# Optimization experiments

Measured on AMD Instinct MI355X. Metric: run time of the kernel, lower is better.

Reference implementation:

```python
import jax, jax.numpy as jnp
import numpy as np

D_MODEL = 512
N_QUBITS = 10
N_LAYERS = 2
N_TOKENS = 16384
DIM = 2 ** N_QUBITS


def _rx(t):
    c = jnp.cos(t / 2) + 0j
    s = -1j * jnp.sin(t / 2)
    return jnp.stack([jnp.stack([c, s]), jnp.stack([s, c])]).astype(jnp.complex64)


def _ry(t):
    c = jnp.cos(t / 2) + 0j
    s = jnp.sin(t / 2) + 0j
    return jnp.stack([jnp.stack([c, -s]), jnp.stack([s, c])]).astype(jnp.complex64)


def _rz(t):
    z = jnp.zeros((), jnp.complex64)
    return jnp.stack([jnp.stack([jnp.exp(-1j * t / 2), z]),
                      jnp.stack([z, jnp.exp(1j * t / 2)])]).astype(jnp.complex64)


def _apply_1q(state, q, U, n):
    # state: [B, 2^n]; qubit 0 is the most significant bit
    B = state.shape[0]
    s = state.reshape(B, 2 ** q, 2, 2 ** (n - q - 1))
    s = jnp.einsum('ij,bajk->baik', U, s)
    return s.reshape(B, 2 ** n)


def _simulate(psi, rot, ent, n):
    # psi: [B, 2^n] complex64. rot: [L, n, 3]. ent: [L, n-1].
    L = rot.shape[0]
    idx = jnp.arange(2 ** n)
    for l in range(L):
        for q in range(n):
            psi = _apply_1q(psi, q, _rx(rot[l, q, 0]), n)
            psi = _apply_1q(psi, q, _ry(rot[l, q, 1]), n)
            psi = _apply_1q(psi, q, _rz(rot[l, q, 2]), n)
        for i in range(n - 1):  # nearest-neighbor parameterized CZ (controlled-phase)
            q1, q2 = i, i + 1
            both = (((idx >> (n - 1 - q1)) & 1) & ((idx >> (n - 1 - q2)) & 1)) == 1
            phase = jnp.where(both, jnp.exp(1j * ent[l, i].astype(jnp.complex64)),
                              jnp.ones((), jnp.complex64))
            psi = psi * phase
    return psi


def setup_inputs() -> dict:
    key = jax.random.key(0)
    ks = jax.random.split(key, 6)
    return {
        'x': jax.random.normal(ks[0], (N_TOKENS, D_MODEL), jnp.float32),
        'W_in': jax.random.normal(ks[1], (DIM, D_MODEL), jnp.float32) / np.sqrt(D_MODEL),
        'b_in': jnp.zeros((DIM,), jnp.float32),
        'W_out': jax.random.normal(ks[2], (D_MODEL, DIM), jnp.float32) / np.sqrt(DIM),
        'b_out': jnp.zeros((D_MODEL,), jnp.float32),
        'rot': jax.random.normal(ks[3], (N_LAYERS, N_QUBITS, 3), jnp.float32),
        'ent': jax.random.normal(ks[4], (N_LAYERS, N_QUBITS - 1), jnp.float32),
        'ln_w': jnp.ones((D_MODEL,), jnp.float32),
        'ln_b': jnp.zeros((D_MODEL,), jnp.float32),
    }


def reference(x, W_in, b_in, W_out, b_out, rot, ent, ln_w, ln_b):
    n = rot.shape[1]
    # input projection to 2^n amplitudes, then L2-normalize (F.normalize, eps=1e-12)
    xq = x @ W_in.T + b_in
    norm = jnp.maximum(jnp.linalg.norm(xq, axis=-1, keepdims=True), 1e-12)
    psi = (xq / norm).astype(jnp.complex64)
    psi = _simulate(psi, rot, ent, n)
    probs = (psi.real ** 2 + psi.imag ** 2).astype(x.dtype)  # |amp|^2
    out = probs @ W_out.T + b_out
    # LayerNorm(d_model), eps=1e-5
    mu = jnp.mean(out, axis=-1, keepdims=True)
    var = jnp.mean((out - mu) ** 2, axis=-1, keepdims=True)
    return (out - mu) / jnp.sqrt(var + 1e-5) * ln_w + ln_b
```

## Files before the change

### kernel.cpp

```cpp
#include <hip/hip_runtime.h>
#include <cstdint>

#define TOKENS 16384
#define DMODEL 512
#define DIM    1024
#define NQ     10
#define NL     2
#define BM     128
#define BN     128
#define BK     32

typedef __bf16 bf16x8 __attribute__((ext_vector_type(8)));
typedef float  f32x4  __attribute__((ext_vector_type(4)));
typedef unsigned short u16x8 __attribute__((ext_vector_type(8)));

__device__ __forceinline__ float b2f(unsigned short h) {
    union { unsigned u; float f; } v; v.u = ((unsigned)h) << 16; return v.f;
}
__device__ __forceinline__ unsigned short f2b(float f) {
    unsigned u = __builtin_bit_cast(unsigned, f);
    return (unsigned short)((u + 0x7FFFu + ((u >> 16) & 1u)) >> 16);
}
__device__ __forceinline__ float2 cmul(float2 a, float2 b) {
    return make_float2(a.x * b.x - a.y * b.y, a.x * b.y + a.y * b.x);
}
__device__ __forceinline__ float2 cadd(float2 a, float2 b) {
    return make_float2(a.x + b.x, a.y + b.y);
}
__device__ __forceinline__ void async_copy16(const void* g, void* l) {
    __builtin_amdgcn_global_load_lds((const __attribute__((address_space(1))) void*)g,
                                     (__attribute__((address_space(3))) void*)l, 16, 0, 0);
}

__global__ __launch_bounds__(256)
void prep_all_kernel(const float* __restrict__ x,  unsigned short* __restrict__ xb,
                     const float* __restrict__ w2, unsigned short* __restrict__ w2b,
                     const float* __restrict__ W_in, unsigned short* __restrict__ wtT,
                     const float* __restrict__ rot, const float* __restrict__ ent,
                     const float* __restrict__ bin,
                     unsigned short* __restrict__ U, float* __restrict__ b2) {
    const int bid = blockIdx.x;
    const int t = threadIdx.x;

    if (bid < 256) {
        __shared__ float2 Gs[NL * NQ * 4];
        const int lane = t & 63;
        const int c = bid * 4 + (t >> 6);

        if (t < NL * NQ) {
            float tx = rot[t * 3 + 0] * 0.5f;
            float ty = rot[t * 3 + 1] * 0.5f;
            float tz = rot[t * 3 + 2] * 0.5f;
            float cx = cosf(tx), sx = sinf(tx);
            float cy = cosf(ty), sy = sinf(ty);
            float cz = cosf(tz), sz = sinf(tz);
            float2 rx00 = make_float2(cx, 0.f),  rx01 = make_float2(0.f, -sx);
            float2 rx10 = make_float2(0.f, -sx), rx11 = make_float2(cx, 0.f);
            float2 ry00 = make_float2(cy, 0.f),  ry01 = make_float2(-sy, 0.f);
            float2 ry10 = make_float2(sy, 0.f),  ry11 = make_float2(cy, 0.f);
            float2 m00 = cadd(cmul(ry00, rx00), cmul(ry01, rx10));
            float2 m01 = cadd(cmul(ry00, rx01), cmul(ry01, rx11));
            float2 m10 = cadd(cmul(ry10, rx00), cmul(ry11, rx10));
            float2 m11 = cadd(cmul(ry10, rx01), cmul(ry11, rx11));
            float2 e0 = make_float2(cz, -sz), e1 = make_float2(cz, sz);
            Gs[t * 4 + 0] = cmul(e0, m00);
            Gs[t * 4 + 1] = cmul(e0, m01);
            Gs[t * 4 + 2] = cmul(e1, m10);
            Gs[t * 4 + 3] = cmul(e1, m11);
        }
        float ef[NL * (NQ - 1)];
        #pragma unroll
        for (int i = 0; i < NL * (NQ - 1); i++) ef[i] = ent[i];
        __syncthreads();

        float2 amp[16];
        #pragma unroll
        for (int r = 0; r < 16; r++)
            amp[r] = make_float2((lane * 16 + r == c) ? 1.f : 0.f, 0.f);

        #pragma unroll 1
        for (int li = 0; li < NL; li++) {
            const int l = NL - 1 - li;
            #pragma unroll
            for (int r = 0; r < 16; r++) {
                int idx = lane * 16 + r;
                float ang = 0.f;
                #pragma unroll
                for (int q = 0; q < NQ - 1; q++) {
                    int both = ((idx >> (9 - q)) & 1) & ((idx >> (8 - q)) & 1);
                    if (both) ang += ef[l * (NQ - 1) + q];
                }
                amp[r] = cmul(amp[r], make_float2(cosf(ang), sinf(ang)));
            }
            const float2* Gl = Gs + l * NQ * 4;
            #pragma unroll
            for (int qq = 0; qq < NQ; qq++) {
                const int q = 9 - qq;
                float2 u00 = Gl[q * 4 + 0], u10 = Gl[q * 4 + 1];
                float2 u01 = Gl[q * 4 + 2], u11 = Gl[q * 4 + 3];
                if (q >= 6) {
                    const int S = 1 << (9 - q);
                    #pragma unroll
                    for (int r = 0; r < 16; r++) {
                        if (r & S) continue;
                        float2 a = amp[r], b = amp[r + S];
                        float2 n0, n1;
                        n0.x = u00.x * a.x - u00.y * a.y + u01.x * b.x - u01.y * b.y;
                        n0.y = u00.x * a.y + u00.y * a.x + u01.x * b.y + u01.y * b.x;
                        n1.x = u10.x * a.x - u10.y * a.y + u11.x * b.x - u11.y * b.y;
                        n1.y = u10.x * a.y + u10.y * a.x + u11.x * b.y + u11.y * b.x;
                        amp[r] = n0; amp[r + S] = n1;
                    }
                } else {
                    const int mask = 32 >> q;
                    int bit = (lane >> (5 - q)) & 1;
                    float2 ua = bit ? u11 : u00;
                    float2 ub = bit ? u10 : u01;
                    #pragma unroll
                    for (int r = 0; r < 16; r++) {
                        float px = __shfl_xor(amp[r].x, mask, 64);
                        float py = __shfl_xor(amp[r].y, mask, 64);
                        float nx = ua.x * amp[r].x - ua.y * amp[r].y + ub.x * px - ub.y * py;
                        float ny = ua.x * amp[r].y + ua.y * amp[r].x + ub.x * py + ub.y * px;
                        amp[r] = make_float2(nx, ny);
                    }
                }
            }
        }

        float accRe = 0.f, accIm = 0.f;
        #pragma unroll
        for (int i = 0; i < 4; i++) {
            float4 bv = *(const float4*)&bin[lane * 16 + i * 4];
            accRe += amp[i * 4 + 0].x * bv.x + amp[i * 4 + 1].x * bv.y
                   + amp[i * 4 + 2].x * bv.z + amp[i * 4 + 3].x * bv.w;
            accIm += amp[i * 4 + 0].y * bv.x + amp[i * 4 + 1].y * bv.y
                   + amp[i * 4 + 2].y * bv.z + amp[i * 4 + 3].y * bv.w;
        }
        #pragma unroll
        for (int m = 1; m < 64; m <<= 1) {
            accRe += __shfl_xor(accRe, m, 64);
            accIm += __shfl_xor(accIm, m, 64);
        }
        if (lane == 0) { b2[2 * c] = accRe; b2[2 * c + 1] = accIm; }

        u16x8 o0, o1, p0, p1;
        #pragma unroll
        for (int r = 0; r < 8; r++) {
            o0[r] = f2b(amp[r].x);     o1[r] = f2b(amp[r + 8].x);
            p0[r] = f2b(amp[r].y);     p1[r] = f2b(amp[r + 8].y);
        }
        unsigned short* rowRe = U + (size_t)(2 * c) * DIM + lane * 16;
        unsigned short* rowIm = U + (size_t)(2 * c + 1) * DIM + lane * 16;
        *(u16x8*)rowRe = o0; *(u16x8*)(rowRe + 8) = o1;
        *(u16x8*)rowIm = p0; *(u16x8*)(rowIm + 8) = p1;
        return;
    }

    if (bid < 768) {
        __shared__ float tile[32][33];
        const int b2i = bid - 256;
        const int tx = t & 31, ty = t >> 5;
        const int d0 = (b2i & 15) * 32, j0 = (b2i >> 4) * 32;
        #pragma unroll
        for (int i = 0; i < 32; i += 8)
            tile[ty + i][tx] = W_in[(size_t)(j0 + ty + i) * DMODEL + d0 + tx];
        __syncthreads();
        #pragma unroll
        for (int i = 0; i < 32; i += 8)
            wtT[(size_t)(d0 + ty + i) * DIM + j0 + tx] = f2b(tile[tx][ty + i]);
        return;
    }

    const int NX4 = TOKENS * DMODEL / 4;
    const int NW4 = DMODEL * DIM / 4;
    const int total = NX4 + NW4;
    const int stride = 2048 * 256;
    for (int i = (bid - 768) * 256 + t; i < total; i += stride) {
        const float* s; unsigned short* d; int j;
        if (i < NX4) { s = x;  d = xb;  j = i; }
        else         { s = w2; d = w2b; j = i - NX4; }
        float4 v = *(const float4*)&s[(size_t)j * 4];
        ushort4 o;
        o.x = f2b(v.x); o.y = f2b(v.y); o.z = f2b(v.z); o.w = f2b(v.w);
        *(ushort4*)&d[(size_t)j * 4] = o;
    }
}

__global__ __launch_bounds__(256)
void fold_kernel(const unsigned short* __restrict__ A, const unsigned short* __restrict__ B,
                 unsigned short* __restrict__ C) {
    __shared__ unsigned short lds_a[BM * BK];
    __shared__ unsigned short lds_b[BN * BK];
    const int t = threadIdx.x;
    const int wave = t >> 6, lane = t & 63;
    const int wm = wave >> 1, wn = wave & 1;
    const int bm0 = blockIdx.y * BM;
    const int bn0 = blockIdx.x * BN;
    const int K = DIM, N = DMODEL;

    f32x4 acc[4][4] = {};
    const int c0 = t, c1 = t + 256;
    const int r0 = c0 >> 2, g0 = (c0 & 3) ^ ((r0 >> 1) & 3);
    const int r1 = c1 >> 2, g1 = (c1 & 3) ^ ((r1 >> 1) & 3);

    for (int k0 = 0; k0 < K; k0 += BK) {
        async_copy16(A + (size_t)(bm0 + r0) * K + k0 + g0 * 8, (char*)lds_a + wave * 1024);
        async_copy16(A + (size_t)(bm0 + r1) * K + k0 + g1 * 8, (char*)lds_a + wave * 1024 + 4096);
        async_copy16(B + (size_t)(bn0 + r0) * K + k0 + g0 * 8, (char*)lds_b + wave * 1024);
        async_copy16(B + (size_t)(bn0 + r1) * K + k0 + g1 * 8, (char*)lds_b + wave * 1024 + 4096);
        __syncthreads();

        bf16x8 af[4], bfr[4];
        #pragma unroll
        for (int i = 0; i < 4; i++) {
            int row = wm * 64 + i * 16 + (lane & 15);
            int slot = (lane >> 4) ^ ((row >> 1) & 3);
            af[i] = *(const bf16x8*)&lds_a[row * BK + slot * 8];
            int nrow = wn * 64 + i * 16 + (lane & 15);
            int nslot = (lane >> 4) ^ ((nrow >> 1) & 3);
            bfr[i] = *(const bf16x8*)&lds_b[nrow * BK + nslot * 8];
        }
        #pragma unroll
        for (int i = 0; i < 4; i++)
            #pragma unroll
            for (int j = 0; j < 4; j++)
                acc[i][j] = __builtin_amdgcn_mfma_f32_16x16x32_bf16(af[i], bfr[j], acc[i][j], 0, 0, 0);
        __syncthreads();
    }

    #pragma unroll
    for (int i = 0; i < 4; i++)
        #pragma unroll
        for (int j = 0; j < 4; j++) {
            int col = bn0 + wn * 64 + j * 16 + (lane & 15);
            #pragma unroll
            for (int r = 0; r < 4; r++) {
                int row = bm0 + wm * 64 + i * 16 + (lane >> 4) * 4 + r;
                C[(size_t)row * N + col] = f2b(acc[i][j][r]);
            }
        }
}

__global__ __launch_bounds__(512, 2)
void gemm1_kernel(const unsigned short* __restrict__ A, const unsigned short* __restrict__ B,
                  const float* __restrict__ bias, unsigned short* __restrict__ P) {
    __shared__ unsigned short sm[2 * 32768];
    const int t = threadIdx.x;
    const int wave = t >> 6, lane = t & 63;
    const int wm = wave >> 2, wn = wave & 3;
    const int laneR = lane & 15;

    const int bid = blockIdx.x;
    const int swz = (bid & 7) * 64 + (bid >> 3);
    const int bm0 = (swz >> 3) * 256;
    const int bn0 = (swz & 7) * 256;

    const int csrc  = (t & 3) ^ ((t >> 3) & 3);
    const int rowg  = t >> 2;
    const unsigned aOff0 = (unsigned)(bm0 + rowg) * DMODEL + csrc * 8;
    const unsigned aOff1 = (unsigned)(bm0 + 128 + rowg) * DMODEL + csrc * 8;
    const unsigned bOff0 = (unsigned)(bn0 + rowg) * DMODEL + csrc * 8;
    const unsigned bOff1 = (unsigned)(bn0 + 128 + rowg) * DMODEL + csrc * 8;

    const int slotc = (((lane >> 4) ^ ((lane >> 1) & 3)) & 3) * 8;

    f32x4 acc[8][4] = {};

    #define G1_STAGE(nbuf, kk, kb)                                                 \
    {                                                                              \
        unsigned short* d0 = sm + (nbuf) * 32768 + (kk) * 8192 + wave * 512;       \
        async_copy16(A + aOff0 + (kb) + (kk) * 32, d0);                            \
        async_copy16(A + aOff1 + (kb) + (kk) * 32, d0 + 4096);                     \
        async_copy16(B + bOff0 + (kb) + (kk) * 32, d0 + 16384);                    \
        async_copy16(B + bOff1 + (kb) + (kk) * 32, d0 + 20480);                    \
    }

    #define G1_COMPUTE(cbuf, kk)                                                   \
    {                                                                              \
        const unsigned short* la = sm + (cbuf) * 32768 + (kk) * 8192;              \
        const unsigned short* lb = la + 16384;                                     \
        bf16x8 af[8], bfr[4];                                                      \
        _Pragma("unroll")                                                          \
        for (int i = 0; i < 8; i++)                                                \
            af[i] = *(const bf16x8*)&la[(wm * 128 + i * 16 + laneR) * 32 + slotc]; \
        _Pragma("unroll")                                                          \
        for (int j = 0; j < 4; j++)                                                \
            bfr[j] = *(const bf16x8*)&lb[(wn * 64 + j * 16 + laneR) * 32 + slotc]; \
        __builtin_amdgcn_s_setprio(1);                                             \
        _Pragma("unroll")                                                          \
        for (int i = 0; i < 8; i++)                                                \
            _Pragma("unroll")                                                      \
            for (int j = 0; j < 4; j++)                                            \
                acc[i][j] = __builtin_amdgcn_mfma_f32_16x16x32_bf16(af[i], bfr[j], acc[i][j], 0, 0, 0); \
        __builtin_amdgcn_s_setprio(0);                                             \
    }

    G1_STAGE(0, 0, 0);
    G1_STAGE(0, 1, 0);
    asm volatile("s_waitcnt vmcnt(4)" ::: "memory");
    asm volatile("s_barrier" ::: "memory");

    #pragma unroll
    for (int kt = 0; kt < 7; kt++) {
        const int cur = kt & 1, nxt = cur ^ 1;
        const unsigned kb = (unsigned)(kt + 1) * 64;
        G1_STAGE(nxt, 0, kb);
        G1_COMPUTE(cur, 0);
        asm volatile("s_waitcnt vmcnt(4)" ::: "memory");
        asm volatile("s_barrier" ::: "memory");
        G1_STAGE(nxt, 1, kb);
        G1_COMPUTE(cur, 1);
        asm volatile("s_waitcnt vmcnt(4)" ::: "memory");
        asm volatile("s_barrier" ::: "memory");
    }
    G1_COMPUTE(1, 0);
    asm volatile("s_waitcnt vmcnt(0)" ::: "memory");
    asm volatile("s_barrier" ::: "memory");
    G1_COMPUTE(1, 1);

    #undef G1_STAGE
    #undef G1_COMPUTE

    #pragma unroll
    for (int i = 0; i < 8; i++) {
        #pragma unroll
        for (int j = 0; j < 4; j++) {
            int col = bn0 + wn * 64 + j * 16 + laneR;
            float bv = bias[col];
            #pragma unroll
            for (int r = 0; r < 4; r++) {
                int row = bm0 + wm * 128 + i * 16 + (lane >> 4) * 4 + r;
                float val = acc[i][j][r] + bv;
                float v2 = val * val;
                float v2p = v2 + __shfl_xor(v2, 1, 64);
                if (!(lane & 1))
                    P[(size_t)row * DIM + (col >> 1)] = f2b(v2p);
            }
        }
    }
}

__global__ __launch_bounds__(256)
void gemm2_ln_kernel(const unsigned short* __restrict__ A,
                     const unsigned short* __restrict__ B,
                     const float* __restrict__ bias,
                     const float* __restrict__ lw, const float* __restrict__ lb,
                     float* __restrict__ out) {
    __shared__ unsigned short lds_a[32 * BK];
    __shared__ unsigned short lds_b[512 * BK];
    __shared__ float redS[4][32], redQ[4][32];
    __shared__ float muS[32], rsS[32], n2s[32];
    const int t = threadIdx.x, wave = t >> 6, lane = t & 63;
    const int bm0 = blockIdx.x * 32;

    f32x4 acc[2][8] = {};
    f32x4 accN[2] = {};
    bf16x8 ones;
    #pragma unroll
    for (int r = 0; r < 8; r++) ones[r] = (__bf16)1.0f;

    const int ra = t >> 2, ga = (t & 3) ^ ((ra >> 1) & 3);

    for (int k0 = 0; k0 < DIM; k0 += BK) {
        if (wave < 2)
            async_copy16(A + (size_t)(bm0 + ra) * DIM + k0 + ga * 8,
                         (char*)lds_a + wave * 1024);
        #pragma unroll
        for (int s = 0; s < 8; s++) {
            int c = t + s * 256;
            int r = c >> 2, g = (c & 3) ^ ((r >> 1) & 3);
            async_copy16(B + (size_t)r * DIM + k0 + g * 8,
                         (char*)lds_b + s * 4096 + wave * 1024);
        }
        __syncthreads();

        bf16x8 af[2], bfr[8];
        #pragma unroll
        for (int i = 0; i < 2; i++) {
            int row = i * 16 + (lane & 15);
            int slot = (lane >> 4) ^ ((row >> 1) & 3);
            af[i] = *(const bf16x8*)&lds_a[row * BK + slot * 8];
        }
        #pragma unroll
        for (int j = 0; j < 8; j++) {
            int nrow = wave * 128 + j * 16 + (lane & 15);
            int nslot = (lane >> 4) ^ ((nrow >> 1) & 3);
            bfr[j] = *(const bf16x8*)&lds_b[nrow * BK + nslot * 8];
        }
        #pragma unroll
        for (int i = 0; i < 2; i++)
            #pragma unroll
            for (int j = 0; j < 8; j++)
                acc[i][j] = __builtin_amdgcn_mfma_f32_16x16x32_bf16(af[i], bfr[j], acc[i][j], 0, 0, 0);
        if (wave == 0) {
            #pragma unroll
            for (int i = 0; i < 2; i++)
                accN[i] = __builtin_amdgcn_mfma_f32_16x16x32_bf16(af[i], ones, accN[i], 0, 0, 0);
        }
        __syncthreads();
    }

    if (wave == 0 && (lane & 15) == 0) {
        #pragma unroll
        for (int i = 0; i < 2; i++)
            #pragma unroll
            for (int r = 0; r < 4; r++)
                n2s[i * 16 + (lane >> 4) * 4 + r] = accN[i][r];
    }
    __syncthreads();

    const int colb = wave * 128;
    float nn[8];
    #pragma unroll
    for (int i = 0; i < 2; i++)
        #pragma unroll
        for (int r = 0; r < 4; r++) {
            int rl = i * 16 + (lane >> 4) * 4 + r;
            nn[i * 4 + r] = 1.0f / fmaxf(n2s[rl], 1e-24f);
        }
    float pS[8], pQ[8];
    #pragma unroll
    for (int i = 0; i < 2; i++)
        #pragma unroll
        for (int r = 0; r < 4; r++) {
            float s = 0.f, q = 0.f;
            #pragma unroll
            for (int j = 0; j < 8; j++) {
                int col = colb + j * 16 + (lane & 15);
                float val = acc[i][j][r] * nn[i * 4 + r] + bias[col];
                acc[i][j][r] = val;
                s += val; q += val * val;
            }
            s += __shfl_xor(s, 1, 64); q += __shfl_xor(q, 1, 64);
            s += __shfl_xor(s, 2, 64); q += __shfl_xor(q, 2, 64);
            s += __shfl_xor(s, 4, 64); q += __shfl_xor(q, 4, 64);
            s += __shfl_xor(s, 8, 64); q += __shfl_xor(q, 8, 64);
            pS[i * 4 + r] = s; pQ[i * 4 + r] = q;
        }
    if ((lane & 15) == 0) {
        #pragma unroll
        for (int i = 0; i < 2; i++)
            #pragma unroll
            for (int r = 0; r < 4; r++) {
                int rl = i * 16 + (lane >> 4) * 4 + r;
                redS[wave][rl] = pS[i * 4 + r];
                redQ[wave][rl] = pQ[i * 4 + r];
            }
    }
    __syncthreads();
    if (t < 32) {
        float s = redS[0][t] + redS[1][t] + redS[2][t] + redS[3][t];
        float q = redQ[0][t] + redQ[1][t] + redQ[2][t] + redQ[3][t];
        float mu = s * (1.0f / DMODEL);
        float var = q * (1.0f / DMODEL) - mu * mu;
        muS[t] = mu;
        rsS[t] = rsqrtf(var + 1e-5f);
    }
    __syncthreads();
    #pragma unroll
    for (int i = 0; i < 2; i++)
        #pragma unroll
        for (int j = 0; j < 8; j++) {
            int col = colb + j * 16 + (lane & 15);
            float w = lw[col], bb = lb[col];
            #pragma unroll
            for (int r = 0; r < 4; r++) {
                int rl = i * 16 + (lane >> 4) * 4 + r;
                out[(size_t)(bm0 + rl) * DMODEL + col] =
                    (acc[i][j][r] - muS[rl]) * rsS[rl] * w + bb;
            }
        }
}

extern "C" void kernel_launch(void* const* d_in, const int* in_sizes, int n_in,
                              void* d_out, int out_size, void* d_ws, size_t ws_size,
                              hipStream_t stream) {
    (void)in_sizes; (void)n_in; (void)out_size; (void)ws_size;
    const float* x     = (const float*)d_in[0];
    const float* W_in  = (const float*)d_in[1];
    const float* b_in  = (const float*)d_in[2];
    const float* W_out = (const float*)d_in[3];
    const float* b_out = (const float*)d_in[4];
    const float* rot   = (const float*)d_in[5];
    const float* ent   = (const float*)d_in[6];
    const float* ln_w  = (const float*)d_in[7];
    const float* ln_b  = (const float*)d_in[8];
    float* out = (float*)d_out;

    char* ws = (char*)d_ws;
    unsigned short* p    = (unsigned short*)ws;
    unsigned short* x_bf = (unsigned short*)(ws + 33554432ull);
    unsigned short* wtT  = (unsigned short*)(ws + 50331648ull);
    unsigned short* w2b  = (unsigned short*)(ws + 51380224ull);
    unsigned short* Ucat = (unsigned short*)(ws + 52428800ull);
    unsigned short* W1c  = (unsigned short*)(ws + 56623104ull);
    float*          b2   = (float*)(ws + 58720256ull);

    prep_all_kernel<<<2816, 256, 0, stream>>>(x, x_bf, W_out, w2b, W_in, wtT,
                                              rot, ent, b_in, Ucat, b2);
    fold_kernel<<<dim3(DMODEL / BN, 2 * DIM / BM), 256, 0, stream>>>(Ucat, wtT, W1c);
    gemm1_kernel<<<512, 512, 0, stream>>>(x_bf, W1c, b2, p);
    gemm2_ln_kernel<<<TOKENS / 32, 256, 0, stream>>>(
        p, w2b, b_out, ln_w, ln_b, out);
}
```

Measured before the change: 224.3 us.

## Restructure gemm1 main loop into four-quadrant ping-pong schedule with deeper prefetch

Rewrites the GEMM1 K-loop as eight 64-wide K tiles. Each tile is processed in four 4x2 MFMA quadrants, with LDS fragment loads interleaved between barriers, and global async loads for tile n+2 are issued into the buffer just consumed. The aim is to overlap LDS reads and global prefetch with MFMA work and to cut register pressure from holding all A/B fragments at once. In exchange it adds many more barriers per K step and adds fragile vmcnt bookkeeping.

After: 219.2 us. 1.02x faster.

```diff
diff --git a/kernel.cpp b/kernel.cpp
--- a/kernel.cpp
+++ b/kernel.cpp
@@ -256,8 +256,8 @@
     const int bm0 = (swz >> 3) * 256;
     const int bn0 = (swz & 7) * 256;
 
-    const int csrc  = (t & 3) ^ ((t >> 3) & 3);
-    const int rowg  = t >> 2;
+    const int csrc = (t & 3) ^ ((t >> 3) & 3);
+    const int rowg = t >> 2;
     const unsigned aOff0 = (unsigned)(bm0 + rowg) * DMODEL + csrc * 8;
     const unsigned aOff1 = (unsigned)(bm0 + 128 + rowg) * DMODEL + csrc * 8;
     const unsigned bOff0 = (unsigned)(bn0 + rowg) * DMODEL + csrc * 8;
@@ -267,60 +267,116 @@
 
     f32x4 acc[8][4] = {};
 
-    #define G1_STAGE(nbuf, kk, kb)                                                 \
-    {                                                                              \
-        unsigned short* d0 = sm + (nbuf) * 32768 + (kk) * 8192 + wave * 512;       \
-        async_copy16(A + aOff0 + (kb) + (kk) * 32, d0);                            \
-        async_copy16(A + aOff1 + (kb) + (kk) * 32, d0 + 4096);                     \
-        async_copy16(B + bOff0 + (kb) + (kk) * 32, d0 + 16384);                    \
-        async_copy16(B + bOff1 + (kb) + (kk) * 32, d0 + 20480);                    \
-    }
-
-    #define G1_COMPUTE(cbuf, kk)                                                   \
-    {                                                                              \
-        const unsigned short* la = sm + (cbuf) * 32768 + (kk) * 8192;              \
-        const unsigned short* lb = la + 16384;                                     \
-        bf16x8 af[8], bfr[4];                                                      \
-        _Pragma("unroll")                                                          \
-        for (int i = 0; i < 8; i++)                                                \
-            af[i] = *(const bf16x8*)&la[(wm * 128 + i * 16 + laneR) * 32 + slotc]; \
-        _Pragma("unroll")                                                          \
-        for (int j = 0; j < 4; j++)                                                \
-            bfr[j] = *(const bf16x8*)&lb[(wn * 64 + j * 16 + laneR) * 32 + slotc]; \
-        __builtin_amdgcn_s_setprio(1);                                             \
-        _Pragma("unroll")                                                          \
-        for (int i = 0; i < 8; i++)                                                \
-            _Pragma("unroll")                                                      \
-            for (int j = 0; j < 4; j++)                                            \
-                acc[i][j] = __builtin_amdgcn_mfma_f32_16x16x32_bf16(af[i], bfr[j], acc[i][j], 0, 0, 0); \
-        __builtin_amdgcn_s_setprio(0);                                             \
-    }
-
-    G1_STAGE(0, 0, 0);
-    G1_STAGE(0, 1, 0);
-    asm volatile("s_waitcnt vmcnt(4)" ::: "memory");
-    asm volatile("s_barrier" ::: "memory");
-
-    #pragma unroll
-    for (int kt = 0; kt < 7; kt++) {
-        const int cur = kt & 1, nxt = cur ^ 1;
-        const unsigned kb = (unsigned)(kt + 1) * 64;
-        G1_STAGE(nxt, 0, kb);
-        G1_COMPUTE(cur, 0);
-        asm volatile("s_waitcnt vmcnt(4)" ::: "memory");
-        asm volatile("s_barrier" ::: "memory");
-        G1_STAGE(nxt, 1, kb);
-        G1_COMPUTE(cur, 1);
-        asm volatile("s_waitcnt vmcnt(4)" ::: "memory");
-        asm volatile("s_barrier" ::: "memory");
-    }
-    G1_COMPUTE(1, 0);
-    asm volatile("s_waitcnt vmcnt(0)" ::: "memory");
-    asm volatile("s_barrier" ::: "memory");
-    G1_COMPUTE(1, 1);
-
-    #undef G1_STAGE
-    #undef G1_COMPUTE
+    #define STAGE_B4(nbuf, tile) {                                        \
+        unsigned short* d = sm + (nbuf) * 32768 + 16384 + wave * 512;     \
+        async_copy16(B + bOff0 + (tile) * 64,      d);                    \
+        async_copy16(B + bOff1 + (tile) * 64,      d + 4096);             \
+        async_copy16(B + bOff0 + (tile) * 64 + 32, d + 8192);             \
+        async_copy16(B + bOff1 + (tile) * 64 + 32, d + 12288);            \
+    }
+    #define STAGE_A4(nbuf, tile) {                                        \
+        unsigned short* d = sm + (nbuf) * 32768 + wave * 512;             \
+        async_copy16(A + aOff0 + (tile) * 64,      d);                    \
+        async_copy16(A + aOff1 + (tile) * 64,      d + 4096);             \
+        async_copy16(A + aOff0 + (tile) * 64 + 32, d + 8192);             \
+        async_copy16(A + aOff1 + (tile) * 64 + 32, d + 12288);            \
+    }
+    #define BARRIER()  asm volatile("s_barrier" ::: "memory")
+
+    STAGE_B4(0, 0); STAGE_A4(0, 0);
+    STAGE_B4(1, 1); STAGE_A4(1, 1);
+    asm volatile("s_waitcnt vmcnt(8)" ::: "memory");
+    BARRIER();
+
+    #pragma unroll
+    for (int n = 0; n < 8; n++) {
+        const int cb = n & 1;
+        const unsigned short* la = sm + cb * 32768;
+        const unsigned short* lb = la + 16384;
+        bf16x8 afv[4][2], bfv[4][2];
+
+        #pragma unroll
+        for (int kk = 0; kk < 2; kk++) {
+            #pragma unroll
+            for (int i = 0; i < 4; i++)
+                afv[i][kk] = *(const bf16x8*)&la[kk * 8192 + (wm * 128 + i * 16 + laneR) * 32 + slotc];
+            #pragma unroll
+            for (int j = 0; j < 2; j++)
+                bfv[j][kk] = *(const bf16x8*)&lb[kk * 8192 + (wn * 64 + j * 16 + laneR) * 32 + slotc];
+        }
+        BARRIER();
+        __builtin_amdgcn_sched_barrier(0);
+        __builtin_amdgcn_s_setprio(1);
+        #pragma unroll
+        for (int i = 0; i < 4; i++)
+            #pragma unroll
+            for (int j = 0; j < 2; j++)
+                #pragma unroll
+                for (int kk = 0; kk < 2; kk++)
+                    acc[i][j] = __builtin_amdgcn_mfma_f32_16x16x32_bf16(afv[i][kk], bfv[j][kk], acc[i][j], 0, 0, 0);
+        __builtin_amdgcn_s_setprio(0);
+        __builtin_amdgcn_sched_barrier(0);
+        BARRIER();
+
+        #pragma unroll
+        for (int kk = 0; kk < 2; kk++)
+            #pragma unroll
+            for (int j = 2; j < 4; j++)
+                bfv[j][kk] = *(const bf16x8*)&lb[kk * 8192 + (wn * 64 + j * 16 + laneR) * 32 + slotc];
+        BARRIER();
+        __builtin_amdgcn_sched_barrier(0);
+        __builtin_amdgcn_s_setprio(1);
+        #pragma unroll
+        for (int i = 0; i < 4; i++)
+            #pragma unroll
+            for (int j = 2; j < 4; j++)
+                #pragma unroll
+                for (int kk = 0; kk < 2; kk++)
+                    acc[i][j] = __builtin_amdgcn_mfma_f32_16x16x32_bf16(afv[i][kk], bfv[j][kk], acc[i][j], 0, 0, 0);
+        __builtin_amdgcn_s_setprio(0);
+        __builtin_amdgcn_sched_barrier(0);
+        BARRIER();
+
+        #pragma unroll
+        for (int kk = 0; kk < 2; kk++)
+            #pragma unroll
+            for (int i = 0; i < 4; i++)
+                afv[i][kk] = *(const bf16x8*)&la[kk * 8192 + (wm * 128 + 64 + i * 16 + laneR) * 32 + slotc];
+        if (n < 6) STAGE_B4(cb, n + 2);
+        BARRIER();
+        __builtin_amdgcn_sched_barrier(0);
+        __builtin_amdgcn_s_setprio(1);
+        #pragma unroll
+        for (int i = 0; i < 4; i++)
+            #pragma unroll
+            for (int j = 2; j < 4; j++)
+                #pragma unroll
+                for (int kk = 0; kk < 2; kk++)
+                    acc[4 + i][j] = __builtin_amdgcn_mfma_f32_16x16x32_bf16(afv[i][kk], bfv[j][kk], acc[4 + i][j], 0, 0, 0);
+        __builtin_amdgcn_s_setprio(0);
+        __builtin_amdgcn_sched_barrier(0);
+        BARRIER();
+
+        if (n < 6) STAGE_A4(cb, n + 2);
+        BARRIER();
+        __builtin_amdgcn_sched_barrier(0);
+        __builtin_amdgcn_s_setprio(1);
+        #pragma unroll
+        for (int i = 0; i < 4; i++)
+            #pragma unroll
+            for (int j = 0; j < 2; j++)
+                #pragma unroll
+                for (int kk = 0; kk < 2; kk++)
+                    acc[4 + i][j] = __builtin_amdgcn_mfma_f32_16x16x32_bf16(afv[i][kk], bfv[j][kk], acc[4 + i][j], 0, 0, 0);
+        __builtin_amdgcn_s_setprio(0);
+        __builtin_amdgcn_sched_barrier(0);
+        if (n < 6)      { asm volatile("s_waitcnt vmcnt(8)" ::: "memory"); }
+        else if (n == 6){ asm volatile("s_waitcnt vmcnt(0)" ::: "memory"); }
+        BARRIER();
+    }
+    #undef STAGE_A4
+    #undef STAGE_B4
+    #undef BARRIER
 
     #pragma unroll
     for (int i = 0; i < 8; i++) {
```

## Double-buffer gemm2 with async pipeline and split re/im rows for gemm1 epilogue

Applied to the files above, without the earlier changes.

Rewrites the second GEMM+LayerNorm kernel to process 64 rows per block with 512 threads and a double-buffered async-copy pipeline with explicit waitcnt/barriers, replacing the single-buffered loop that synchronized twice per K step. It also reorders the folded unitary rows so real and imaginary parts land 16 columns apart. This lets the gemm1 epilogue compute |amp|^2 within a lane instead of using a cross-lane shuffle and half-lane stores. The aim is to overlap global loads with MFMA work and cut epilogue shuffles, at the cost of more LDS per block and lower occupancy.

After: 202.5 us. 1.11x faster.

```diff
diff --git a/kernel.cpp b/kernel.cpp
--- a/kernel.cpp
+++ b/kernel.cpp
@@ -142,7 +142,8 @@
             accRe += __shfl_xor(accRe, m, 64);
             accIm += __shfl_xor(accIm, m, 64);
         }
-        if (lane == 0) { b2[2 * c] = accRe; b2[2 * c + 1] = accIm; }
+        const int nR = ((c >> 4) << 5) + (c & 15);
+        if (lane == 0) { b2[nR] = accRe; b2[nR + 16] = accIm; }
 
         u16x8 o0, o1, p0, p1;
         #pragma unroll
@@ -150,8 +151,8 @@
             o0[r] = f2b(amp[r].x);     o1[r] = f2b(amp[r + 8].x);
             p0[r] = f2b(amp[r].y);     p1[r] = f2b(amp[r + 8].y);
         }
-        unsigned short* rowRe = U + (size_t)(2 * c) * DIM + lane * 16;
-        unsigned short* rowIm = U + (size_t)(2 * c + 1) * DIM + lane * 16;
+        unsigned short* rowRe = U + (size_t)nR * DIM + lane * 16;
+        unsigned short* rowIm = U + (size_t)(nR + 16) * DIM + lane * 16;
         *(u16x8*)rowRe = o0; *(u16x8*)(rowRe + 8) = o1;
         *(u16x8*)rowIm = p0; *(u16x8*)(rowIm + 8) = p1;
         return;
@@ -245,6 +246,7 @@
 __global__ __launch_bounds__(512, 2)
 void gemm1_kernel(const unsigned short* __restrict__ A, const unsigned short* __restrict__ B,
                   const float* __restrict__ bias, unsigned short* __restrict__ P) {
+    const int K = DMODEL;
     __shared__ unsigned short sm[2 * 32768];
     const int t = threadIdx.x;
     const int wave = t >> 6, lane = t & 63;
@@ -256,8 +258,8 @@
     const int bm0 = (swz >> 3) * 256;
     const int bn0 = (swz & 7) * 256;
 
-    const int csrc  = (t & 3) ^ ((t >> 3) & 3);
-    const int rowg  = t >> 2;
+    const int csrc = (t & 3) ^ ((t >> 3) & 3);
+    const int rowg = t >> 2;
     const unsigned aOff0 = (unsigned)(bm0 + rowg) * DMODEL + csrc * 8;
     const unsigned aOff1 = (unsigned)(bm0 + 128 + rowg) * DMODEL + csrc * 8;
     const unsigned bOff0 = (unsigned)(bn0 + rowg) * DMODEL + csrc * 8;
@@ -301,6 +303,7 @@
     asm volatile("s_waitcnt vmcnt(4)" ::: "memory");
     asm volatile("s_barrier" ::: "memory");
 
+    const int NT = K / 64;
     #pragma unroll
     for (int kt = 0; kt < 7; kt++) {
         const int cur = kt & 1, nxt = cur ^ 1;
@@ -318,6 +321,7 @@
     asm volatile("s_waitcnt vmcnt(0)" ::: "memory");
     asm volatile("s_barrier" ::: "memory");
     G1_COMPUTE(1, 1);
+    (void)NT;
 
     #undef G1_STAGE
     #undef G1_COMPUTE
@@ -325,34 +329,41 @@
     #pragma unroll
     for (int i = 0; i < 8; i++) {
         #pragma unroll
-        for (int j = 0; j < 4; j++) {
-            int col = bn0 + wn * 64 + j * 16 + laneR;
-            float bv = bias[col];
+        for (int jp = 0; jp < 2; jp++) {
+            int colRe = bn0 + wn * 64 + jp * 32 + laneR;
+            float bRe = bias[colRe];
+            float bIm = bias[colRe + 16];
+            int pc = (bn0 >> 1) + wn * 32 + jp * 16 + laneR;
             #pragma unroll
             for (int r = 0; r < 4; r++) {
                 int row = bm0 + wm * 128 + i * 16 + (lane >> 4) * 4 + r;
-                float val = acc[i][j][r] + bv;
-                float v2 = val * val;
-                float v2p = v2 + __shfl_xor(v2, 1, 64);
-                if (!(lane & 1))
-                    P[(size_t)row * DIM + (col >> 1)] = f2b(v2p);
+                float vr = acc[i][2 * jp][r] + bRe;
+                float vi = acc[i][2 * jp + 1][r] + bIm;
+                P[(size_t)row * DIM + pc] = f2b(vr * vr + vi * vi);
             }
         }
     }
 }
 
-__global__ __launch_bounds__(256)
+__global__ __launch_bounds__(512)
 void gemm2_ln_kernel(const unsigned short* __restrict__ A,
                      const unsigned short* __restrict__ B,
                      const float* __restrict__ bias,
                      const float* __restrict__ lw, const float* __restrict__ lb,
                      float* __restrict__ out) {
-    __shared__ unsigned short lds_a[32 * BK];
-    __shared__ unsigned short lds_b[512 * BK];
-    __shared__ float redS[4][32], redQ[4][32];
-    __shared__ float muS[32], rsS[32], n2s[32];
+    __shared__ unsigned short sm[2 * 36864];
+    __shared__ float redS[4][64], redQ[4][64];
+    __shared__ float muS[64], rsS[64], n2s[64];
     const int t = threadIdx.x, wave = t >> 6, lane = t & 63;
-    const int bm0 = blockIdx.x * 32;
+    const int wm = wave >> 2, wn = wave & 3;
+    const int laneR = lane & 15;
+    const int bm0 = blockIdx.x * 64;
+
+    const int csrc = (t & 3) ^ ((t >> 3) & 3);
+    const int akk  = t >> 8, arow = (t >> 2) & 63;
+    const unsigned aSrc = (unsigned)(bm0 + arow) * DIM + akk * 32 + csrc * 8;
+    const int brow = t >> 2;
+    const int slotc = (((lane >> 4) ^ ((lane >> 1) & 3)) & 3) * 8;
 
     f32x4 acc[2][8] = {};
     f32x4 accN[2] = {};
@@ -360,75 +371,90 @@
     #pragma unroll
     for (int r = 0; r < 8; r++) ones[r] = (__bf16)1.0f;
 
-    const int ra = t >> 2, ga = (t & 3) ^ ((ra >> 1) & 3);
-
-    for (int k0 = 0; k0 < DIM; k0 += BK) {
-        if (wave < 2)
-            async_copy16(A + (size_t)(bm0 + ra) * DIM + k0 + ga * 8,
-                         (char*)lds_a + wave * 1024);
-        #pragma unroll
-        for (int s = 0; s < 8; s++) {
-            int c = t + s * 256;
-            int r = c >> 2, g = (c & 3) ^ ((r >> 1) & 3);
-            async_copy16(B + (size_t)r * DIM + k0 + g * 8,
-                         (char*)lds_b + s * 4096 + wave * 1024);
-        }
-        __syncthreads();
-
-        bf16x8 af[2], bfr[8];
-        #pragma unroll
-        for (int i = 0; i < 2; i++) {
-            int row = i * 16 + (lane & 15);
-            int slot = (lane >> 4) ^ ((row >> 1) & 3);
-            af[i] = *(const bf16x8*)&lds_a[row * BK + slot * 8];
-        }
-        #pragma unroll
-        for (int j = 0; j < 8; j++) {
-            int nrow = wave * 128 + j * 16 + (lane & 15);
-            int nslot = (lane >> 4) ^ ((nrow >> 1) & 3);
-            bfr[j] = *(const bf16x8*)&lds_b[nrow * BK + nslot * 8];
-        }
+    #define G2_STAGE_A(nbuf, kb) {                                          \
+        async_copy16(A + aSrc + (kb), sm + (nbuf) * 36864 + t * 8);         \
+    }
+    #define G2_STAGE_B(nbuf, kk, kb) {                                      \
+        unsigned short* d = sm + (nbuf) * 36864 + 4096 + (kk) * 16384 + t * 8; \
+        const unsigned short* s0 = B + (size_t)brow * DIM + (kb) + (kk) * 32 + csrc * 8; \
+        async_copy16(s0,                 d);                                 \
+        async_copy16(s0 + 128 * DIM,     d + 4096);                         \
+        async_copy16(s0 + 256 * DIM,     d + 8192);                         \
+        async_copy16(s0 + 384 * DIM,     d + 12288);                        \
+    }
+    #define G2_COMPUTE(cbuf, kk) {                                          \
+        const unsigned short* la  = sm + (cbuf) * 36864 + (kk) * 2048;      \
+        const unsigned short* lbp = sm + (cbuf) * 36864 + 4096 + (kk) * 16384; \
+        bf16x8 af[2], bfr[8];                                               \
+        _Pragma("unroll")                                                   \
+        for (int i = 0; i < 2; i++)                                         \
+            af[i] = *(const bf16x8*)&la[(wm * 32 + i * 16 + laneR) * 32 + slotc]; \
+        _Pragma("unroll")                                                   \
+        for (int j = 0; j < 8; j++)                                         \
+            bfr[j] = *(const bf16x8*)&lbp[(wn * 128 + j * 16 + laneR) * 32 + slotc]; \
+        __builtin_amdgcn_s_setprio(1);                                      \
+        _Pragma("unroll")                                                   \
+        for (int i = 0; i < 2; i++)                                         \
+            _Pragma("unroll")                                               \
+            for (int j = 0; j < 8; j++)                                     \
+                acc[i][j] = __builtin_amdgcn_mfma_f32_16x16x32_bf16(af[i], bfr[j], acc[i][j], 0, 0, 0); \
+        if (wn == 0) {                                                      \
+            _Pragma("unroll")                                               \
+            for (int i = 0; i < 2; i++)                                     \
+                accN[i] = __builtin_amdgcn_mfma_f32_16x16x32_bf16(af[i], ones, accN[i], 0, 0, 0); \
+        }                                                                   \
+        __builtin_amdgcn_s_setprio(0);                                      \
+    }
+
+    G2_STAGE_A(0, 0); G2_STAGE_B(0, 0, 0); G2_STAGE_B(0, 1, 0);
+    asm volatile("s_waitcnt vmcnt(4)" ::: "memory");
+    asm volatile("s_barrier" ::: "memory");
+
+    #pragma unroll
+    for (int n = 0; n < 15; n++) {
+        const int cb = n & 1, nb = cb ^ 1;
+        const unsigned kb = (unsigned)(n + 1) * 64;
+        G2_STAGE_A(nb, kb); G2_STAGE_B(nb, 0, kb);
+        G2_COMPUTE(cb, 0);
+        asm volatile("s_waitcnt vmcnt(5)" ::: "memory");
+        asm volatile("s_barrier" ::: "memory");
+        G2_STAGE_B(nb, 1, kb);
+        G2_COMPUTE(cb, 1);
+        asm volatile("s_waitcnt vmcnt(4)" ::: "memory");
+        asm volatile("s_barrier" ::: "memory");
+    }
+    G2_COMPUTE(1, 0);
+    asm volatile("s_waitcnt vmcnt(0)" ::: "memory");
+    asm volatile("s_barrier" ::: "memory");
+    G2_COMPUTE(1, 1);
+
+    #undef G2_STAGE_A
+    #undef G2_STAGE_B
+    #undef G2_COMPUTE
+
+    if (wn == 0 && laneR == 0) {
         #pragma unroll
         for (int i = 0; i < 2; i++)
             #pragma unroll
-            for (int j = 0; j < 8; j++)
-                acc[i][j] = __builtin_amdgcn_mfma_f32_16x16x32_bf16(af[i], bfr[j], acc[i][j], 0, 0, 0);
-        if (wave == 0) {
-            #pragma unroll
-            for (int i = 0; i < 2; i++)
-                accN[i] = __builtin_amdgcn_mfma_f32_16x16x32_bf16(af[i], ones, accN[i], 0, 0, 0);
-        }
-        __syncthreads();
-    }
-
-    if (wave == 0 && (lane & 15) == 0) {
-        #pragma unroll
-        for (int i = 0; i < 2; i++)
-            #pragma unroll
             for (int r = 0; r < 4; r++)
-                n2s[i * 16 + (lane >> 4) * 4 + r] = accN[i][r];
+                n2s[wm * 32 + i * 16 + (lane >> 4) * 4 + r] = accN[i][r];
     }
     __syncthreads();
 
-    const int colb = wave * 128;
-    float nn[8];
+    float bvj[8];
+    #pragma unroll
+    for (int j = 0; j < 8; j++) bvj[j] = bias[wn * 128 + j * 16 + laneR];
+
     #pragma unroll
     for (int i = 0; i < 2; i++)
         #pragma unroll
         for (int r = 0; r < 4; r++) {
-            int rl = i * 16 + (lane >> 4) * 4 + r;
-            nn[i * 4 + r] = 1.0f / fmaxf(n2s[rl], 1e-24f);
-        }
-    float pS[8], pQ[8];
-    #pragma unroll
-    for (int i = 0; i < 2; i++)
-        #pragma unroll
-        for (int r = 0; r < 4; r++) {
+            int rl = wm * 32 + i * 16 + (lane >> 4) * 4 + r;
+            float nn = 1.0f / fmaxf(n2s[rl], 1e-24f);
             float s = 0.f, q = 0.f;
             #pragma unroll
             for (int j = 0; j < 8; j++) {
-                int col = colb + j * 16 + (lane & 15);
-                float val = acc[i][j][r] * nn[i * 4 + r] + bias[col];
+                float val = acc[i][j][r] * nn + bvj[j];
                 acc[i][j][r] = val;
                 s += val; q += val * val;
             }
@@ -436,20 +462,10 @@
             s += __shfl_xor(s, 2, 64); q += __shfl_xor(q, 2, 64);
             s += __shfl_xor(s, 4, 64); q += __shfl_xor(q, 4, 64);
             s += __shfl_xor(s, 8, 64); q += __shfl_xor(q, 8, 64);
-            pS[i * 4 + r] = s; pQ[i * 4 + r] = q;
-        }
-    if ((lane & 15) == 0) {
-        #pragma unroll
-        for (int i = 0; i < 2; i++)
-            #pragma unroll
-            for (int r = 0; r < 4; r++) {
-                int rl = i * 16 + (lane >> 4) * 4 + r;
-                redS[wave][rl] = pS[i * 4 + r];
-                redQ[wave][rl] = pQ[i * 4 + r];
-            }
-    }
+            if (laneR == 0) { redS[wn][rl] = s; redQ[wn][rl] = q; }
+        }
     __syncthreads();
-    if (t < 32) {
+    if (t < 64) {
         float s = redS[0][t] + redS[1][t] + redS[2][t] + redS[3][t];
         float q = redQ[0][t] + redQ[1][t] + redQ[2][t] + redQ[3][t];
         float mu = s * (1.0f / DMODEL);
@@ -462,11 +478,11 @@
     for (int i = 0; i < 2; i++)
         #pragma unroll
         for (int j = 0; j < 8; j++) {
-            int col = colb + j * 16 + (lane & 15);
+            int col = wn * 128 + j * 16 + laneR;
             float w = lw[col], bb = lb[col];
             #pragma unroll
             for (int r = 0; r < 4; r++) {
-                int rl = i * 16 + (lane >> 4) * 4 + r;
+                int rl = wm * 32 + i * 16 + (lane >> 4) * 4 + r;
                 out[(size_t)(bm0 + rl) * DMODEL + col] =
                     (acc[i][j][r] - muS[rl]) * rsS[rl] * w + bb;
             }
@@ -501,6 +517,6 @@
                                               rot, ent, b_in, Ucat, b2);
     fold_kernel<<<dim3(DMODEL / BN, 2 * DIM / BM), 256, 0, stream>>>(Ucat, wtT, W1c);
     gemm1_kernel<<<512, 512, 0, stream>>>(x_bf, W1c, b2, p);
-    gemm2_ln_kernel<<<TOKENS / 32, 256, 0, stream>>>(
+    gemm2_ln_kernel<<<TOKENS / 64, 512, 0, stream>>>(
         p, w2b, b_out, ln_w, ln_b, out);
 }
```
